# Kernel optimization log

Hardware: AMD Instinct MI355X
Metric: run time of the kernel (lower is better)

Reference implementation:

```python
import jax, jax.numpy as jnp
import numpy as np

B, H, L, T, V = 256, 512, 3, 200, 100  # batch, hidden, lstm layers, decode steps (text_max_len-1), vocab


def setup_inputs() -> dict:
    key = jax.random.key(0)
    ks = jax.random.split(key, 12)
    s = 0.04  # ~1/sqrt(512), keeps gates in a sane range like trained weights
    return {
        "feat": jax.random.normal(ks[0], (B, H), jnp.float32),
        "visual_w": jax.random.normal(ks[1], (H, H), jnp.float32) * s,
        "visual_b": jax.random.normal(ks[2], (H,), jnp.float32) * s,
        "embed": jax.random.normal(ks[3], (V, H), jnp.float32),
        "w_ih": jax.random.normal(ks[4], (L, 4 * H, H), jnp.float32) * s,
        "w_hh": jax.random.normal(ks[5], (L, 4 * H, H), jnp.float32) * s,
        "b_ih": jax.random.normal(ks[6], (L, 4 * H), jnp.float32) * s,
        "b_hh": jax.random.normal(ks[7], (L, 4 * H), jnp.float32) * s,
        "proj_w1": jax.random.normal(ks[8], (2 * H, H), jnp.float32) * s,
        "proj_b1": jax.random.normal(ks[9], (2 * H,), jnp.float32) * s,
        "proj_w2": jax.random.normal(ks[10], (V, 2 * H), jnp.float32) * s,
        "proj_b2": jax.random.normal(ks[11], (V,), jnp.float32) * s,
        "start_idx": 1,  # tokenizer.char2idx[sos_token]
    }


def _lstm_stack_step(h, c, x, w_ih, w_hh, b_ih, b_hh):
    # h, c: [L, B, H]; x: [B, H]. PyTorch gate order: i, f, g, o.
    hs, cs = [], []
    for l in range(L):
        gates = x @ w_ih[l].T + b_ih[l] + h[l] @ w_hh[l].T + b_hh[l]  # [B, 4H]
        i, f, g, o = jnp.split(gates, 4, axis=-1)
        c_new = jax.nn.sigmoid(f) * c[l] + jax.nn.sigmoid(i) * jnp.tanh(g)
        h_new = jax.nn.sigmoid(o) * jnp.tanh(c_new)
        hs.append(h_new)
        cs.append(c_new)
        x = h_new  # inter-layer dropout is identity in eval mode
    return jnp.stack(hs), jnp.stack(cs), x


def reference(feat, visual_w, visual_b, embed, w_ih, w_hh, b_ih, b_hh,
              proj_w1, proj_b1, proj_w2, proj_b2, start_idx):
    # encoder feature -> visual_proj (applied once in forward, once more in _init_hidden)
    feat1 = feat @ visual_w.T + visual_b
    h0_layer = feat1 @ visual_w.T + visual_b           # same weights for every layer
    h0 = jnp.broadcast_to(h0_layer, (L, B, H))
    c0 = jnp.zeros((L, B, H), jnp.float32)
    x0 = jnp.broadcast_to(embed[start_idx], (B, H))    # embedded <sos>

    def step(carry, _):
        h, c, x = carry
        h, c, top = _lstm_stack_step(h, c, x, w_ih, w_hh, b_ih, b_hh)
        # next input is the top-layer output, detached (inp = out[-1:].detach())
        return (h, c, jax.lax.stop_gradient(top)), top

    (_, _, _), outs = jax.lax.scan(step, (h0, c0, x0), None, length=T)  # outs: [T, B, H]
    res = outs.transpose(1, 0, 2)                                       # [B, T, H]
    hmid = jax.nn.gelu(res @ proj_w1.T + proj_b1, approximate=False)    # [B, T, 2H]
    logits = hmid @ proj_w2.T + proj_b2                                  # [B, T, V]
    return logits.transpose(0, 2, 1)                                     # [B, V, T]
```

## Files before the change

### kernel.cpp

```cpp
#include <hip/hip_runtime.h>
#include <hip/hip_bf16.h>
#include <hip/hip_fp16.h>

#define NB 256
#define NH 512
#define NL 3
#define NT 200
#define NV 100
#define NVP 112
#define NG 2048
#define NK 1024
#define NS (NT * NL)

using f16x8 = __attribute__((ext_vector_type(8))) _Float16;
using f32x4 = __attribute__((ext_vector_type(4))) float;
using u32x4 = __attribute__((ext_vector_type(4))) unsigned int;

__device__ __forceinline__ float sigf(float x) { return 1.f / (1.f + __expf(-x)); }
__device__ __forceinline__ float tanhf_(float x) { return 2.f / (1.f + __expf(-2.f * x)) - 1.f; }

__global__ void k_probe(int* __restrict__ rowmap, int* __restrict__ colmap) {
  const int lane = threadIdx.x & 63;
  f16x8 a, b;
  const _Float16 idv = (_Float16)(float)(lane & 15);
  const _Float16 inv = (_Float16)(1.f / 32.f);
#pragma unroll
  for (int j = 0; j < 8; ++j) { a[j] = idv; b[j] = inv; }
  f32x4 d = {0.f, 0.f, 0.f, 0.f};
  d = __builtin_amdgcn_mfma_f32_16x16x32_f16(a, b, d, 0, 0, 0);
#pragma unroll
  for (int r = 0; r < 4; ++r) rowmap[lane * 4 + r] = (int)(d[r] + 0.5f);
#pragma unroll
  for (int j = 0; j < 8; ++j) { a[j] = inv; b[j] = idv; }
  f32x4 e = {0.f, 0.f, 0.f, 0.f};
  e = __builtin_amdgcn_mfma_f32_16x16x32_f16(a, b, e, 0, 0, 0);
#pragma unroll
  for (int r = 0; r < 4; ++r) colmap[lane * 4 + r] = (int)(e[r] + 0.5f);
}

__global__ void k_prep_w(const float* __restrict__ w_ih, const float* __restrict__ w_hh,
                         const float* __restrict__ b_ih, const float* __restrict__ b_hh,
                         _Float16* __restrict__ Wih, _Float16* __restrict__ Whh,
                         float* __restrict__ bias) {
  const int stride = gridDim.x * blockDim.x;
  const int tid0 = blockIdx.x * blockDim.x + threadIdx.x;
  for (int idx = tid0; idx < NL * NG * NH; idx += stride) {
    const int k = idx & (NH - 1);
    const int r = (idx >> 9) & (NG - 1);
    const int l = idx >> 20;
    const int hu = r >> 2, g = r & 3;
    const size_t soff = ((size_t)(l * NG + g * NH + hu)) * NH + k;
    Wih[idx] = (_Float16)w_ih[soff];
    Whh[idx] = (_Float16)w_hh[soff];
  }
  for (int idx = tid0; idx < NL * NG; idx += stride) {
    const int r = idx & (NG - 1);
    const int l = idx >> 11;
    const int hu = r >> 2, g = r & 3;
    const int srow = l * NG + g * NH + hu;
    bias[idx] = b_ih[srow] + b_hh[srow];
  }
}

__global__ void k_prep_misc(const float* __restrict__ embed, const int* __restrict__ start_idx,
                            const float* __restrict__ w1, const float* __restrict__ b1,
                            const float* __restrict__ w2, const float* __restrict__ b2,
                            _Float16* __restrict__ x0, _Float16* __restrict__ pw1, float* __restrict__ pb1,
                            _Float16* __restrict__ pw2, float* __restrict__ pb2, int* __restrict__ flags) {
  const int stride = gridDim.x * blockDim.x;
  const int tid0 = blockIdx.x * blockDim.x + threadIdx.x;
  for (int i = tid0; i < 256 * 16; i += stride) flags[i] = 0;
  const int st = start_idx[0];
  for (int i = tid0; i < NB * NH; i += stride)
    x0[i] = (_Float16)embed[(size_t)st * NH + (i & (NH - 1))];
  for (int i = tid0; i < 2 * NH * NH; i += stride)
    pw1[i] = (_Float16)w1[i];
  for (int i = tid0; i < NVP * NK; i += stride) {
    const int r = i >> 10;
    pw2[i] = (_Float16)((r < NV) ? w2[i] : 0.f);
  }
  for (int i = tid0; i < 2 * NH; i += stride) pb1[i] = b1[i];
  for (int i = tid0; i < NVP; i += stride) pb2[i] = (i < NV) ? b2[i] : 0.f;
}

__global__ void k_gemv512(const float* __restrict__ x, const float* __restrict__ w,
                          const float* __restrict__ bias, float* __restrict__ out) {
  const int b = blockIdx.x;
  __shared__ float xs[NH];
  for (int i = threadIdx.x; i < NH; i += 256) xs[i] = x[(size_t)b * NH + i];
  __syncthreads();
  const int wave = threadIdx.x >> 6, lane = threadIdx.x & 63;
  for (int j = wave; j < NH; j += 4) {
    const float* wr = w + (size_t)j * NH;
    float s = 0.f;
#pragma unroll
    for (int i = 0; i < 8; ++i) s += wr[lane + i * 64] * xs[lane + i * 64];
#pragma unroll
    for (int o = 32; o > 0; o >>= 1) s += __shfl_down(s, o);
    if (lane == 0) out[(size_t)b * NH + j] = s + bias[j];
  }
}

__global__ void k_gemv2_h0(const float* __restrict__ feat1, const float* __restrict__ w,
                           const float* __restrict__ bias, _Float16* __restrict__ h0b) {
  const int b = blockIdx.x;
  __shared__ float xs[NH];
  for (int i = threadIdx.x; i < NH; i += 256) xs[i] = feat1[(size_t)b * NH + i];
  __syncthreads();
  const int wave = threadIdx.x >> 6, lane = threadIdx.x & 63;
  for (int j = wave; j < NH; j += 4) {
    const float* wr = w + (size_t)j * NH;
    float s = 0.f;
#pragma unroll
    for (int i = 0; i < 8; ++i) s += wr[lane + i * 64] * xs[lane + i * 64];
#pragma unroll
    for (int o = 32; o > 0; o >>= 1) s += __shfl_down(s, o);
    if (lane == 0) h0b[(size_t)b * NH + j] = (_Float16)(s + bias[j]);
  }
}

__global__ __launch_bounds__(512, 2) void k_lstm(const _Float16* __restrict__ Wih,
                                                 const _Float16* __restrict__ Whh,
                                                 const float* __restrict__ bias,
                                                 _Float16* hx, const _Float16* __restrict__ h0b,
                                                 const _Float16* __restrict__ x0,
                                                 _Float16* __restrict__ outs,
                                                 const int* __restrict__ rowmap,
                                                 const int* __restrict__ colmap,
                                                 int* flags) {
  const int tid = threadIdx.x;
  const int lane = tid & 63;
  const int wave = tid >> 6;
  const int bid = blockIdx.x;
  const int jj = bid & 31;
  const int bm = bid >> 5;
  const int bn = (jj & 7) * 4 + (jj >> 3);
  const int gbase = bm * 32;
  const int grp = wave >> 2;
  const int wn = wave & 3;
  const int lr = lane & 15;
  const int lh = lane >> 4;
  const int nb0 = bn * 64 + wn * 16;
  __shared__ _Float16 Als[32][512];
  __shared__ float gl[32][68];
  __shared__ float pend[3][32][68];
  __shared__ _Float16 hout[32][16];

  int rm[4], cm[4];
#pragma unroll
  for (int r = 0; r < 4; ++r) {
    rm[r] = rowmap[lane * 4 + r];
    cm[r] = colmap[lane * 4 + r];
  }
  const int bl_ = tid >> 4;
  const int hu = tid & 15;
  float creg[NL] = {0.f, 0.f, 0.f};
  float bsv[NL][4];
#pragma unroll
  for (int l = 0; l < NL; ++l)
#pragma unroll
    for (int g = 0; g < 4; ++g) bsv[l][g] = bias[l * NG + (bn * 16 + hu) * 4 + g];

  f16x8 wreg[16];

#define PREFETCH(LX, LZ)                                                          \
  do {                                                                            \
    const _Float16* wb = (grp == 0)                                               \
        ? (Wih + ((size_t)((LX) * NG + nb0 + lr)) * NH + lh * 8)                  \
        : (Whh + ((size_t)((LZ) * NG + nb0 + lr)) * NH + lh * 8);                 \
    _Pragma("unroll") for (int k_ = 0; k_ < 16; ++k_)                             \
        wreg[k_] = *(const f16x8*)(wb + k_ * 32);                                 \
  } while (0)

#define AREAD0(KK) (*(const f16x8*)&Als[lr][(((KK) * 4 + lh) ^ (lr & 7)) * 8])
#define AREAD1(KK) (*(const f16x8*)&Als[16 + lr][(((KK) * 4 + lh) ^ (lr & 7)) * 8])

#define GEMM_TO(DST)                                                              \
  do {                                                                            \
    f32x4 a0_ = {0.f, 0.f, 0.f, 0.f}, a1_ = {0.f, 0.f, 0.f, 0.f};                 \
    _Pragma("unroll") for (int kk = 0; kk < 16; ++kk) {                           \
      f16x8 av0 = AREAD0(kk);                                                     \
      f16x8 av1 = AREAD1(kk);                                                     \
      a0_ = __builtin_amdgcn_mfma_f32_16x16x32_f16(av0, wreg[kk], a0_, 0, 0, 0);  \
      a1_ = __builtin_amdgcn_mfma_f32_16x16x32_f16(av1, wreg[kk], a1_, 0, 0, 0);  \
    }                                                                             \
    _Pragma("unroll") for (int r = 0; r < 4; ++r) {                               \
      (DST)[rm[r]][wn * 16 + cm[r]] = a0_[r];                                     \
      (DST)[16 + rm[r]][wn * 16 + cm[r]] = a1_[r];                                \
    }                                                                             \
  } while (0)

#define STAGE_A(SRC, VOLQ)                                                        \
  do {                                                                            \
    _Pragma("unroll") for (int c = 0; c < 4; ++c) {                               \
      const int i_ = tid + c * 512;                                               \
      const int rr = i_ >> 6, cc = i_ & 63;                                       \
      u32x4 v_ = *(const VOLQ u32x4*)((SRC) + (size_t)(bm * 32 + rr) * NH + cc * 8); \
      *(u32x4*)&Als[rr][(cc ^ (rr & 7)) * 8] = v_;                                \
    }                                                                             \
  } while (0)

  STAGE_A(h0b, );
  __syncthreads();
  if (grp == 0) {
#pragma unroll 1
    for (int lp = 0; lp < 3; ++lp) {
      const _Float16* bp = Whh + ((size_t)(lp * NG + nb0 + lr)) * NH + lh * 8;
      f32x4 a0 = {0.f, 0.f, 0.f, 0.f}, a1 = {0.f, 0.f, 0.f, 0.f};
#pragma unroll 4
      for (int kk = 0; kk < 16; ++kk) {
        f16x8 av0 = AREAD0(kk);
        f16x8 av1 = AREAD1(kk);
        f16x8 bv = *(const f16x8*)(bp + (size_t)kk * 32);
        a0 = __builtin_amdgcn_mfma_f32_16x16x32_f16(av0, bv, a0, 0, 0, 0);
        a1 = __builtin_amdgcn_mfma_f32_16x16x32_f16(av1, bv, a1, 0, 0, 0);
      }
#pragma unroll
      for (int r = 0; r < 4; ++r) {
        pend[lp][rm[r]][wn * 16 + cm[r]] = a0[r];
        pend[lp][16 + rm[r]][wn * 16 + cm[r]] = a1[r];
      }
    }
  }
  PREFETCH(0, 2);
  __syncthreads();
  STAGE_A(x0, );
  __syncthreads();

#pragma unroll 1
  for (int t = 0; t < NT; ++t) {
#pragma unroll
    for (int l = 0; l < NL; ++l) {
      const int s = t * 3 + l;
      if (grp == 0) {
        GEMM_TO(gl);
      } else if (s >= 1 && s <= NS - 3) {
        GEMM_TO(pend[(l + 2) % 3]);
      }
      PREFETCH((l + 1) % 3, l);
      __syncthreads();
      {
        const f32x4 gx = *(const f32x4*)&gl[bl_][hu * 4];
        const f32x4 gh = *(const f32x4*)&pend[l][bl_][hu * 4];
        const float gi = gx[0] + gh[0] + bsv[l][0];
        const float gf = gx[1] + gh[1] + bsv[l][1];
        const float gg = gx[2] + gh[2] + bsv[l][2];
        const float go = gx[3] + gh[3] + bsv[l][3];
        const float cn = sigf(gf) * creg[l] + sigf(gi) * tanhf_(gg);
        const float hn = sigf(go) * tanhf_(cn);
        creg[l] = cn;
        hout[bl_][hu] = (_Float16)hn;
      }
      __syncthreads();
      if (wave == 0) {
        const int row = lane >> 1, half = lane & 1;
        _Float16* dst = hx + (size_t)(s & 1) * NB * NH + (size_t)(bm * 32 + row) * NH + bn * 16 + half * 8;
        u32x4 v = *(const u32x4*)&hout[row][half * 8];
        *(volatile u32x4*)dst = v;
        asm volatile("s_waitcnt vmcnt(0)" ::: "memory");
        if (lane == 0) *(volatile int*)&flags[(gbase + jj) * 16] = s + 1;
      }
      if (wave == 1 && l == 2) {
        const int row = lane >> 1, half = lane & 1;
        _Float16* dst = outs + ((size_t)t * NB + bm * 32 + row) * NH + bn * 16 + half * 8;
        *(u32x4*)dst = *(const u32x4*)&hout[row][half * 8];
      }
      if (s < NS - 1) {
        if (lane < 32) {
          const volatile int* fp = (const volatile int*)&flags[(gbase + lane) * 16];
          while (*fp < s + 1) __builtin_amdgcn_s_sleep(1);
        }
        STAGE_A(hx + (size_t)(s & 1) * NB * NH, volatile);
        __syncthreads();
      }
    }
  }
#undef STAGE_A
#undef GEMM_TO
#undef AREAD0
#undef AREAD1
#undef PREFETCH
}

__global__ __launch_bounds__(256) void k_proj(const _Float16* __restrict__ outs, const _Float16* __restrict__ pw1,
                                              const float* __restrict__ pb1, const _Float16* __restrict__ pw2,
                                              const float* __restrict__ pb2,
                                              const int* __restrict__ rowmap, const int* __restrict__ colmap,
                                              float* __restrict__ out) {
  const int tid = threadIdx.x;
  const int lane = tid & 63;
  const int wave = tid >> 6;
  const int lr = lane & 15;
  const int lh = lane >> 4;
  const int mbase = blockIdx.x * 16;
  __shared__ _Float16 hm[16][NK + 8];
  int rm[4], cm[4];
#pragma unroll
  for (int r = 0; r < 4; ++r) {
    rm[r] = rowmap[lane * 4 + r];
    cm[r] = colmap[lane * 4 + r];
  }
  const int mrow = mbase + lr;
  const _Float16* ap = outs + ((size_t)(mrow % NT) * NB + (mrow / NT)) * NH + lh * 8;
  for (int nf = 0; nf < 16; ++nf) {
    const int n0 = wave * 256 + nf * 16;
    f32x4 acc = {0.f, 0.f, 0.f, 0.f};
    const _Float16* bp = pw1 + (size_t)(n0 + lr) * NH + lh * 8;
#pragma unroll 4
    for (int kk = 0; kk < 16; ++kk) {
      f16x8 a = *(const f16x8*)(ap + kk * 32);
      f16x8 b = *(const f16x8*)(bp + kk * 32);
      acc = __builtin_amdgcn_mfma_f32_16x16x32_f16(a, b, acc, 0, 0, 0);
    }
#pragma unroll
    for (int r = 0; r < 4; ++r) {
      const float v = acc[r] + pb1[n0 + cm[r]];
      const float gv = 0.5f * v * (1.f + erff(v * 0.70710678118654752f));
      hm[rm[r]][n0 + cm[r]] = (_Float16)gv;
    }
  }
  __syncthreads();
  for (int nf = wave; nf < 7; nf += 4) {
    const int n0 = nf * 16;
    f32x4 acc = {0.f, 0.f, 0.f, 0.f};
    const _Float16* bp = pw2 + (size_t)(n0 + lr) * NK + lh * 8;
#pragma unroll 4
    for (int kk = 0; kk < 32; ++kk) {
      f16x8 a = *(const f16x8*)(&hm[lr][kk * 32 + lh * 8]);
      f16x8 b = *(const f16x8*)(bp + kk * 32);
      acc = __builtin_amdgcn_mfma_f32_16x16x32_f16(a, b, acc, 0, 0, 0);
    }
#pragma unroll
    for (int r = 0; r < 4; ++r) {
      const int v = n0 + cm[r];
      if (v < NV) {
        const int m = mbase + rm[r];
        out[((size_t)(m / NT) * NV + v) * NT + (m % NT)] = acc[r] + pb2[v];
      }
    }
  }
}

extern "C" void kernel_launch(void* const* d_in, const int* in_sizes, int n_in,
                              void* d_out, int out_size, void* d_ws, size_t ws_size,
                              hipStream_t stream) {
  const float* feat = (const float*)d_in[0];
  const float* visual_w = (const float*)d_in[1];
  const float* visual_b = (const float*)d_in[2];
  const float* embed = (const float*)d_in[3];
  const float* w_ih = (const float*)d_in[4];
  const float* w_hh = (const float*)d_in[5];
  const float* b_ih = (const float*)d_in[6];
  const float* b_hh = (const float*)d_in[7];
  const float* proj_w1 = (const float*)d_in[8];
  const float* proj_b1 = (const float*)d_in[9];
  const float* proj_w2 = (const float*)d_in[10];
  const float* proj_b2 = (const float*)d_in[11];
  const int* start_idx = (const int*)d_in[12];
  float* out = (float*)d_out;

  char* ws = (char*)d_ws;
  size_t off = 0;
  auto alloc = [&](size_t bytes) -> void* {
    void* p = ws + off;
    off += (bytes + 255) & ~(size_t)255;
    return p;
  };
  _Float16* Wih = (_Float16*)alloc((size_t)NL * NG * NH * 2);
  _Float16* Whh = (_Float16*)alloc((size_t)NL * NG * NH * 2);
  float* bias = (float*)alloc((size_t)NL * NG * 4);
  _Float16* hx = (_Float16*)alloc((size_t)2 * NB * NH * 2);
  _Float16* h0b = (_Float16*)alloc((size_t)NB * NH * 2);
  _Float16* x0 = (_Float16*)alloc((size_t)NB * NH * 2);
  _Float16* outsb = (_Float16*)alloc((size_t)NT * NB * NH * 2);
  float* feat1 = (float*)alloc((size_t)NB * NH * 4);
  _Float16* pw1 = (_Float16*)alloc((size_t)2 * NH * NH * 2);
  _Float16* pw2 = (_Float16*)alloc((size_t)NVP * NK * 2);
  float* pb1 = (float*)alloc((size_t)2 * NH * 4);
  float* pb2 = (float*)alloc((size_t)NVP * 4);
  int* flags = (int*)alloc(256 * 16 * 4);
  int* rowmap = (int*)alloc(256 * 4);
  int* colmap = (int*)alloc(256 * 4);
  if (off > ws_size) return;

  k_probe<<<dim3(1), dim3(64), 0, stream>>>(rowmap, colmap);
  k_prep_w<<<dim3(2048), dim3(256), 0, stream>>>(w_ih, w_hh, b_ih, b_hh, Wih, Whh, bias);
  k_prep_misc<<<dim3(1024), dim3(256), 0, stream>>>(embed, start_idx, proj_w1, proj_b1, proj_w2, proj_b2,
                                                    x0, pw1, pb1, pw2, pb2, flags);
  k_gemv512<<<dim3(NB), dim3(256), 0, stream>>>(feat, visual_w, visual_b, feat1);
  k_gemv2_h0<<<dim3(NB), dim3(256), 0, stream>>>(feat1, visual_w, visual_b, h0b);
  k_lstm<<<dim3(256), dim3(512), 0, stream>>>(Wih, Whh, bias, hx, h0b, x0, outsb, rowmap, colmap, flags);
  k_proj<<<dim3(3200), dim3(256), 0, stream>>>(outsb, pw1, pb1, pw2, pb2, rowmap, colmap, out);
}
```

Before: 5.090 ms.

## Split K across wave groups and defer hidden-state GEMM off critical path

Before, the 8 waves were split into two groups: one did the input GEMM (Wih) and the other the recurrent GEMM (Whh), each over the full K=512. Now every wave does both GEMMs over half of K and writes partial sums that are added in the gate epilogue. The Whh GEMM for the next step now runs after the h output is published but before the flag is set, and the weight prefetch moves later. The aim is to halve the critical-path GEMM latency before the first sync. The cost is more registers (A fragments held in registers), double the LDS partial buffers, and extra additions in the epilogue.

```diff
diff --git a/kernel.cpp b/kernel.cpp
--- a/kernel.cpp
+++ b/kernel.cpp
@@ -136,14 +136,14 @@
   const int bm = bid >> 5;
   const int bn = (jj & 7) * 4 + (jj >> 3);
   const int gbase = bm * 32;
-  const int grp = wave >> 2;
   const int wn = wave & 3;
+  const int kh = wave >> 2;
   const int lr = lane & 15;
   const int lh = lane >> 4;
   const int nb0 = bn * 64 + wn * 16;
   __shared__ _Float16 Als[32][512];
-  __shared__ float gl[32][68];
-  __shared__ float pend[3][32][68];
+  __shared__ float gl[2][32][68];
+  __shared__ float pend[3][2][32][68];
   __shared__ _Float16 hout[32][16];
 
   int rm[4], cm[4];
@@ -161,32 +161,24 @@
 #pragma unroll
     for (int g = 0; g < 4; ++g) bsv[l][g] = bias[l * NG + (bn * 16 + hu) * 4 + g];
 
-  f16x8 wreg[16];
+  f16x8 wx[8], wh[8], areg[16];
 
 #define PREFETCH(LX, LZ)                                                          \
   do {                                                                            \
-    const _Float16* wb = (grp == 0)                                               \
-        ? (Wih + ((size_t)((LX) * NG + nb0 + lr)) * NH + lh * 8)                  \
-        : (Whh + ((size_t)((LZ) * NG + nb0 + lr)) * NH + lh * 8);                 \
-    _Pragma("unroll") for (int k_ = 0; k_ < 16; ++k_)                             \
-        wreg[k_] = *(const f16x8*)(wb + k_ * 32);                                 \
+    const _Float16* wbx = Wih + ((size_t)((LX) * NG + nb0 + lr)) * NH + kh * 256 + lh * 8; \
+    const _Float16* wbh = Whh + ((size_t)((LZ) * NG + nb0 + lr)) * NH + kh * 256 + lh * 8; \
+    _Pragma("unroll") for (int k_ = 0; k_ < 8; ++k_) {                            \
+      wx[k_] = *(const f16x8*)(wbx + k_ * 32);                                    \
+      wh[k_] = *(const f16x8*)(wbh + k_ * 32);                                    \
+    }                                                                             \
   } while (0)
 
-#define AREAD0(KK) (*(const f16x8*)&Als[lr][(((KK) * 4 + lh) ^ (lr & 7)) * 8])
-#define AREAD1(KK) (*(const f16x8*)&Als[16 + lr][(((KK) * 4 + lh) ^ (lr & 7)) * 8])
-
-#define GEMM_TO(DST)                                                              \
+#define LOAD_AREG()                                                               \
   do {                                                                            \
-    f32x4 a0_ = {0.f, 0.f, 0.f, 0.f}, a1_ = {0.f, 0.f, 0.f, 0.f};                 \
-    _Pragma("unroll") for (int kk = 0; kk < 16; ++kk) {                           \
-      f16x8 av0 = AREAD0(kk);                                                     \
-      f16x8 av1 = AREAD1(kk);                                                     \
-      a0_ = __builtin_amdgcn_mfma_f32_16x16x32_f16(av0, wreg[kk], a0_, 0, 0, 0);  \
-      a1_ = __builtin_amdgcn_mfma_f32_16x16x32_f16(av1, wreg[kk], a1_, 0, 0, 0);  \
-    }                                                                             \
-    _Pragma("unroll") for (int r = 0; r < 4; ++r) {                               \
-      (DST)[rm[r]][wn * 16 + cm[r]] = a0_[r];                                     \
-      (DST)[16 + rm[r]][wn * 16 + cm[r]] = a1_[r];                                \
+    _Pragma("unroll") for (int kk = 0; kk < 8; ++kk) {                            \
+      const int c_ = kh * 32 + kk * 4 + lh;                                       \
+      areg[kk] = *(const f16x8*)&Als[lr][(c_ ^ (lr & 7)) * 8];                    \
+      areg[8 + kk] = *(const f16x8*)&Als[16 + lr][(c_ ^ (lr & 7)) * 8];           \
     }                                                                             \
   } while (0)
 
@@ -202,24 +194,23 @@
 
   STAGE_A(h0b, );
   __syncthreads();
-  if (grp == 0) {
+  LOAD_AREG();
 #pragma unroll 1
-    for (int lp = 0; lp < 3; ++lp) {
-      const _Float16* bp = Whh + ((size_t)(lp * NG + nb0 + lr)) * NH + lh * 8;
-      f32x4 a0 = {0.f, 0.f, 0.f, 0.f}, a1 = {0.f, 0.f, 0.f, 0.f};
-#pragma unroll 4
-      for (int kk = 0; kk < 16; ++kk) {
-        f16x8 av0 = AREAD0(kk);
-        f16x8 av1 = AREAD1(kk);
-        f16x8 bv = *(const f16x8*)(bp + (size_t)kk * 32);
-        a0 = __builtin_amdgcn_mfma_f32_16x16x32_f16(av0, bv, a0, 0, 0, 0);
-        a1 = __builtin_amdgcn_mfma_f32_16x16x32_f16(av1, bv, a1, 0, 0, 0);
-      }
-#pragma unroll
-      for (int r = 0; r < 4; ++r) {
-        pend[lp][rm[r]][wn * 16 + cm[r]] = a0[r];
-        pend[lp][16 + rm[r]][wn * 16 + cm[r]] = a1[r];
-      }
+  for (int lp = 0; lp < 3; ++lp) {
+    const _Float16* wbh = Whh + ((size_t)(lp * NG + nb0 + lr)) * NH + kh * 256 + lh * 8;
+    f16x8 wt[8];
+#pragma unroll
+    for (int k_ = 0; k_ < 8; ++k_) wt[k_] = *(const f16x8*)(wbh + k_ * 32);
+    f32x4 a0 = {0.f, 0.f, 0.f, 0.f}, a1 = {0.f, 0.f, 0.f, 0.f};
+#pragma unroll
+    for (int kk = 0; kk < 8; ++kk) {
+      a0 = __builtin_amdgcn_mfma_f32_16x16x32_f16(areg[kk], wt[kk], a0, 0, 0, 0);
+      a1 = __builtin_amdgcn_mfma_f32_16x16x32_f16(areg[8 + kk], wt[kk], a1, 0, 0, 0);
+    }
+#pragma unroll
+    for (int r = 0; r < 4; ++r) {
+      pend[lp][kh][rm[r]][wn * 16 + cm[r]] = a0[r];
+      pend[lp][kh][16 + rm[r]][wn * 16 + cm[r]] = a1[r];
     }
   }
   PREFETCH(0, 2);
@@ -232,20 +223,30 @@
 #pragma unroll
     for (int l = 0; l < NL; ++l) {
       const int s = t * 3 + l;
-      if (grp == 0) {
-        GEMM_TO(gl);
-      } else if (s >= 1 && s <= NS - 3) {
-        GEMM_TO(pend[(l + 2) % 3]);
-      }
-      PREFETCH((l + 1) % 3, l);
+      LOAD_AREG();
+      {
+        f32x4 a0 = {0.f, 0.f, 0.f, 0.f}, a1 = {0.f, 0.f, 0.f, 0.f};
+#pragma unroll
+        for (int kk = 0; kk < 8; ++kk) {
+          a0 = __builtin_amdgcn_mfma_f32_16x16x32_f16(areg[kk], wx[kk], a0, 0, 0, 0);
+          a1 = __builtin_amdgcn_mfma_f32_16x16x32_f16(areg[8 + kk], wx[kk], a1, 0, 0, 0);
+        }
+#pragma unroll
+        for (int r = 0; r < 4; ++r) {
+          gl[kh][rm[r]][wn * 16 + cm[r]] = a0[r];
+          gl[kh][16 + rm[r]][wn * 16 + cm[r]] = a1[r];
+        }
+      }
       __syncthreads();
       {
-        const f32x4 gx = *(const f32x4*)&gl[bl_][hu * 4];
-        const f32x4 gh = *(const f32x4*)&pend[l][bl_][hu * 4];
-        const float gi = gx[0] + gh[0] + bsv[l][0];
-        const float gf = gx[1] + gh[1] + bsv[l][1];
-        const float gg = gx[2] + gh[2] + bsv[l][2];
-        const float go = gx[3] + gh[3] + bsv[l][3];
+        const f32x4 gx0 = *(const f32x4*)&gl[0][bl_][hu * 4];
+        const f32x4 gx1 = *(const f32x4*)&gl[1][bl_][hu * 4];
+        const f32x4 gh0 = *(const f32x4*)&pend[l][0][bl_][hu * 4];
+        const f32x4 gh1 = *(const f32x4*)&pend[l][1][bl_][hu * 4];
+        const float gi = gx0[0] + gx1[0] + gh0[0] + gh1[0] + bsv[l][0];
+        const float gf = gx0[1] + gx1[1] + gh0[1] + gh1[1] + bsv[l][1];
+        const float gg = gx0[2] + gx1[2] + gh0[2] + gh1[2] + bsv[l][2];
+        const float go = gx0[3] + gx1[3] + gh0[3] + gh1[3] + bsv[l][3];
         const float cn = sigf(gf) * creg[l] + sigf(gi) * tanhf_(gg);
         const float hn = sigf(go) * tanhf_(cn);
         creg[l] = cn;
@@ -257,6 +258,22 @@
         _Float16* dst = hx + (size_t)(s & 1) * NB * NH + (size_t)(bm * 32 + row) * NH + bn * 16 + half * 8;
         u32x4 v = *(const u32x4*)&hout[row][half * 8];
         *(volatile u32x4*)dst = v;
+      }
+      if (s >= 1 && s <= NS - 3) {
+        const int l2 = (l + 2) % 3;
+        f32x4 a0 = {0.f, 0.f, 0.f, 0.f}, a1 = {0.f, 0.f, 0.f, 0.f};
+#pragma unroll
+        for (int kk = 0; kk < 8; ++kk) {
+          a0 = __builtin_amdgcn_mfma_f32_16x16x32_f16(areg[kk], wh[kk], a0, 0, 0, 0);
+          a1 = __builtin_amdgcn_mfma_f32_16x16x32_f16(areg[8 + kk], wh[kk], a1, 0, 0, 0);
+        }
+#pragma unroll
+        for (int r = 0; r < 4; ++r) {
+          pend[l2][kh][rm[r]][wn * 16 + cm[r]] = a0[r];
+          pend[l2][kh][16 + rm[r]][wn * 16 + cm[r]] = a1[r];
+        }
+      }
+      if (wave == 0) {
         asm volatile("s_waitcnt vmcnt(0)" ::: "memory");
         if (lane == 0) *(volatile int*)&flags[(gbase + jj) * 16] = s + 1;
       }
@@ -266,6 +283,7 @@
         *(u32x4*)dst = *(const u32x4*)&hout[row][half * 8];
       }
       if (s < NS - 1) {
+        PREFETCH((l + 1) % 3, l);
         if (lane < 32) {
           const volatile int* fp = (const volatile int*)&flags[(gbase + lane) * 16];
           while (*fp < s + 1) __builtin_amdgcn_s_sleep(1);
@@ -276,9 +294,7 @@
     }
   }
 #undef STAGE_A
-#undef GEMM_TO
-#undef AREAD0
-#undef AREAD1
+#undef LOAD_AREG
 #undef PREFETCH
 }
 
```

After: 4.791 ms. -5.9%, faster.
